# Kernel optimization log

Hardware: AMD Instinct MI355X
Metric: run time of the kernel (lower is better)

Reference implementation:

```python
import jax, jax.numpy as jnp
import numpy as np

N_HEADS = 16
ROPE_BASE = 10000.0


def _apply_rope(t, cos, sin):
    # t: (B, H, S, D); cos/sin: (S, D/2). Rotate-half convention.
    d2 = t.shape[-1] // 2
    t1, t2 = t[..., :d2], t[..., d2:]
    return jnp.concatenate([t1 * cos - t2 * sin, t2 * cos + t1 * sin], axis=-1)


def setup_inputs() -> dict:
    key = jax.random.key(0)
    k0, k1, k2, k3, k4 = jax.random.split(key, 5)
    B, S, E = 4, 2048, 1024
    scale = 0.02
    x = jax.random.normal(k0, (B, S, E), dtype=jnp.float32)
    w_qkv = jax.random.normal(k1, (E, 3 * E), dtype=jnp.float32) * scale
    b_qkv = jnp.zeros((3 * E,), dtype=jnp.float32)
    w_proj = jax.random.normal(k2, (E, E), dtype=jnp.float32) * scale
    b_proj = jnp.zeros((E,), dtype=jnp.float32)
    return {"x": x, "w_qkv": w_qkv, "b_qkv": b_qkv, "w_proj": w_proj, "b_proj": b_proj}


def reference(x, w_qkv, b_qkv, w_proj, b_proj):
    B, S, E = x.shape
    H = N_HEADS
    D = E // H
    # fused QKV projection
    qkv = x @ w_qkv + b_qkv                      # (B, S, 3E)
    q, k, v = jnp.split(qkv, 3, axis=-1)
    def to_heads(t):
        return t.reshape(B, S, H, D).transpose(0, 2, 1, 3)  # (B, H, S, D)
    q, k, v = to_heads(q), to_heads(k), to_heads(v)
    # RoPE (rotate-half)
    inv_freq = ROPE_BASE ** (-jnp.arange(0, D, 2, dtype=jnp.float32) / D)  # (D/2,)
    pos = jnp.arange(S, dtype=jnp.float32)
    freqs = pos[:, None] * inv_freq[None, :]     # (S, D/2)
    cos, sin = jnp.cos(freqs), jnp.sin(freqs)
    q = _apply_rope(q, cos, sin)
    k = _apply_rope(k, cos, sin)
    # causal SDPA
    scores = jnp.einsum('bhqd,bhkd->bhqk', q, k) / jnp.sqrt(jnp.float32(D))
    causal = jnp.tril(jnp.ones((S, S), dtype=bool))
    scores = jnp.where(causal, scores, jnp.float32(-1e30))
    probs = jax.nn.softmax(scores, axis=-1)
    out = jnp.einsum('bhqk,bhkd->bhqd', probs, v)  # (B, H, S, D)
    out = out.transpose(0, 2, 1, 3).reshape(B, S, E)
    # output projection (dropout is identity at p=0 / eval)
    return out @ w_proj + b_proj
```

## Files before the change

kernel.cpp:

```cpp
#include <hip/hip_runtime.h>

typedef unsigned short u16;
typedef __bf16 bf16x8 __attribute__((ext_vector_type(8)));
typedef float f32x4 __attribute__((ext_vector_type(4)));

__device__ __forceinline__ u16 f2b(float f) {
    unsigned u = __builtin_bit_cast(unsigned, f);
    unsigned r = (u + 0x7fffu + ((u >> 16) & 1u)) >> 16;
    return (u16)r;
}
#if __has_builtin(__builtin_amdgcn_cvt_pk_bf16_f32)
typedef __bf16 bf16x2_t __attribute__((ext_vector_type(2)));
__device__ __forceinline__ unsigned pk2(float a, float b) {
    return __builtin_bit_cast(unsigned, __builtin_amdgcn_cvt_pk_bf16_f32(a, b));
}
#else
__device__ __forceinline__ unsigned pk2(float a, float b) {
    return (unsigned)f2b(a) | ((unsigned)f2b(b) << 16);
}
#endif
#if __has_builtin(__builtin_amdgcn_exp2f)
#define EXP2F(x) __builtin_amdgcn_exp2f(x)
#else
#define EXP2F(x) exp2f(x)
#endif

__device__ __forceinline__ void gl_lds16(const u16* g, u16* l) {
    __builtin_amdgcn_global_load_lds(
        (const __attribute__((address_space(1))) unsigned*)(const void*)g,
        (__attribute__((address_space(3))) unsigned*)(void*)l, 16, 0, 0);
}

__global__ __launch_bounds__(256) void k_convert(const float* __restrict__ in,
                                                 u16* __restrict__ out, int n8) {
    int i = blockIdx.x * 256 + threadIdx.x;
    if (i >= n8) return;
    const float4* p = (const float4*)(in + (size_t)i * 8);
    float4 a = p[0], b = p[1];
    u16 t[8] = {f2b(a.x), f2b(a.y), f2b(a.z), f2b(a.w),
                f2b(b.x), f2b(b.y), f2b(b.z), f2b(b.w)};
    *(uint4*)(out + (size_t)i * 8) = *(const uint4*)t;
}

__global__ __launch_bounds__(256) void k_transpose_bf16(const float* __restrict__ in,
                                                        u16* __restrict__ out,
                                                        int R, int C) {
    __shared__ u16 tile[64][72];
    int tc = blockIdx.x * 64;
    int tr = blockIdx.y * 64;
    for (int i = threadIdx.x; i < 4096; i += 256) {
        int r = i >> 6, c = i & 63;
        tile[c][r] = f2b(in[(size_t)(tr + r) * C + tc + c]);
    }
    __syncthreads();
    for (int i = threadIdx.x; i < 4096; i += 256) {
        int r = i >> 6, c = i & 63;
        out[(size_t)(tc + r) * R + tr + c] = tile[r][c];
    }
}

__device__ __forceinline__ void gemm_mainloop(const u16* __restrict__ Ab,
                                              const u16* __restrict__ Bb, int K,
                                              u16* As, u16* Bs, int tid,
                                              f32x4 (&acc)[4][4]) {
    const int wave = tid >> 6, lane = tid & 63;
    const int col = lane & 15, quad = lane >> 4;
    const int wm = wave >> 1, wn = wave & 1;
    const int lrow = lane >> 2, lk = (lane & 3) * 8;
    u16* ldsA0 = As + (wave * 16) * 32;
    u16* ldsA1 = As + (64 + wave * 16) * 32;
    u16* ldsB0 = Bs + (wave * 16) * 32;
    u16* ldsB1 = Bs + (64 + wave * 16) * 32;
    const u16* gA0 = Ab + (size_t)(wave * 16 + lrow) * K + lk;
    const u16* gA1 = gA0 + (size_t)64 * K;
    const u16* gB0 = Bb + (size_t)(wave * 16 + lrow) * K + lk;
    const u16* gB1 = gB0 + (size_t)64 * K;
    for (int k0 = 0; k0 < K; k0 += 64) {
        if (k0) __syncthreads();
#pragma unroll
        for (int kh = 0; kh < 2; ++kh) {
            int ko = k0 + kh * 32;
            gl_lds16(gA0 + ko, ldsA0 + kh * 4096);
            gl_lds16(gA1 + ko, ldsA1 + kh * 4096);
            gl_lds16(gB0 + ko, ldsB0 + kh * 4096);
            gl_lds16(gB1 + ko, ldsB1 + kh * 4096);
        }
        __syncthreads();
#pragma unroll
        for (int kh = 0; kh < 2; ++kh) {
            bf16x8 af[4], bfr[4];
#pragma unroll
            for (int mt = 0; mt < 4; ++mt)
                af[mt] = *(const bf16x8*)(As + kh * 4096 +
                                          (wm * 64 + mt * 16 + col) * 32 + quad * 8);
#pragma unroll
            for (int nt = 0; nt < 4; ++nt)
                bfr[nt] = *(const bf16x8*)(Bs + kh * 4096 +
                                           (wn * 64 + nt * 16 + col) * 32 + quad * 8);
#pragma unroll
            for (int mt = 0; mt < 4; ++mt)
#pragma unroll
                for (int nt = 0; nt < 4; ++nt)
                    acc[mt][nt] = __builtin_amdgcn_mfma_f32_16x16x32_bf16(
                        af[mt], bfr[nt], acc[mt][nt], 0, 0, 0);
        }
    }
}

__global__ __launch_bounds__(256) void k_gemm_qkv_rope(
    const u16* __restrict__ A, const u16* __restrict__ Bt,
    const float* __restrict__ bias, u16* __restrict__ Qr, u16* __restrict__ Kr,
    u16* __restrict__ Vt) {
    __shared__ __align__(16) u16 As[2 * 128 * 32];
    __shared__ __align__(16) u16 Bs[2 * 128 * 32];
    const int K = 1024;
    int tid = threadIdx.x;
    int lane = tid & 63, wave = tid >> 6;
    int col = lane & 15, quad = lane >> 4;
    int wm = wave >> 1, wn = wave & 1;
    int mBase = blockIdx.y * 128;
    int nBase = blockIdx.x * 128;
    f32x4 acc[4][4] = {};
    gemm_mainloop(A + (size_t)mBase * K, Bt + (size_t)nBase * K, K, As, Bs, tid, acc);

    int n64 = nBase + wn * 64;
    int region = n64 >> 10;
    int h = (n64 & 1023) >> 6;
    if (region < 2) {
        u16* out = (region == 0) ? Qr : Kr;
        float qs = (region == 0) ? 0.18033688011112042f : 1.0f;
        const float C0 = 0.4152410118609203f;
#pragma unroll
        for (int nt = 0; nt < 2; ++nt) {
            int d1 = nt * 16 + col;
            float inv_freq = exp2f(-C0 * (float)d1);
            float b1 = bias[n64 + nt * 16 + col];
            float b2 = bias[n64 + nt * 16 + col + 32];
#pragma unroll
            for (int mt = 0; mt < 4; ++mt) {
                int mrow = mBase + wm * 64 + mt * 16 + quad * 4;
#pragma unroll
                for (int r = 0; r < 4; ++r) {
                    int m = mrow + r;
                    int s = m & 2047, b = m >> 11;
                    float sn, cs;
                    sincosf((float)s * inv_freq, &sn, &cs);
                    float t1 = acc[mt][nt][r] + b1;
                    float t2 = acc[mt][nt + 2][r] + b2;
                    size_t base = ((size_t)((b * 16 + h) * 2048 + s)) * 64;
                    out[base + d1] = f2b((t1 * cs - t2 * sn) * qs);
                    out[base + d1 + 32] = f2b((t2 * cs + t1 * sn) * qs);
                }
            }
        }
    } else {
#pragma unroll
        for (int nt = 0; nt < 4; ++nt) {
            int d = nt * 16 + col;
            float bv = bias[n64 + nt * 16 + col];
#pragma unroll
            for (int mt = 0; mt < 4; ++mt) {
                int mrow = mBase + wm * 64 + mt * 16 + quad * 4;
#pragma unroll
                for (int r = 0; r < 4; ++r) {
                    int m = mrow + r;
                    int s = m & 2047, b = m >> 11;
                    Vt[((size_t)((b * 16 + h) * 64 + d)) * 2048 + s] =
                        f2b(acc[mt][nt][r] + bv);
                }
            }
        }
    }
}

__global__ __launch_bounds__(256) void k_attn(const u16* __restrict__ Qr,
                                              const u16* __restrict__ Kr,
                                              const u16* __restrict__ Vt,
                                              u16* __restrict__ O) {
    __shared__ __align__(16) u16 Ks[64 * 72];
    __shared__ __align__(16) u16 Vs[64 * 72];
    int tid = threadIdx.x, wave = tid >> 6, lane = tid & 63;
    int col = lane & 15, quad = lane >> 4;
    int bx = blockIdx.x, bh = blockIdx.y;
    int b = bh >> 4, h = bh & 15;
    size_t headQ = (size_t)bh * 2048 * 64;
    size_t headV = (size_t)bh * 64 * 2048;
    int r0 = tid >> 3, kc = tid & 7;
    int rb72 = ((col >> 2) * 8 + (col & 3)) * 72;

    for (int half = 0; half < 2; ++half) {
        int qb = half ? bx : (15 - bx);
        int t0 = 2 * qb, t1 = t0 + 1;
        int myq0 = qb * 128 + wave * 16 + col;
        int myq1 = myq0 + 64;
        const u16* qp0 = Qr + headQ + (size_t)myq0 * 64;
        const u16* qp1 = Qr + headQ + (size_t)myq1 * 64;
        bf16x8 aq00 = *(const bf16x8*)(qp0 + quad * 8);
        bf16x8 aq01 = *(const bf16x8*)(qp0 + 32 + quad * 8);
        bf16x8 aq10 = *(const bf16x8*)(qp1 + quad * 8);
        bf16x8 aq11 = *(const bf16x8*)(qp1 + 32 + quad * 8);
        f32x4 o0[4] = {}, o1[4] = {};
        float l0 = 0.f, l1 = 0.f;

        for (int j = 0; j <= t1; ++j) {
            bool d0 = (j <= t0);
            __syncthreads();
            {
                const u16* kg = Kr + headQ + (size_t)(j * 64 + r0) * 64 + kc * 8;
                const u16* vg = Vt + headV + (size_t)r0 * 2048 + j * 64 + kc * 8;
                *(uint4*)(Ks + r0 * 72 + kc * 8) = *(const uint4*)kg;
                *(uint4*)(Ks + (r0 + 32) * 72 + kc * 8) = *(const uint4*)(kg + 32 * 64);
                *(uint4*)(Vs + r0 * 72 + kc * 8) = *(const uint4*)vg;
                *(uint4*)(Vs + (r0 + 32) * 72 + kc * 8) = *(const uint4*)(vg + 32 * 2048);
            }
            __syncthreads();
            f32x4 s0[4], s1[4];
#pragma unroll
            for (int nt = 0; nt < 4; ++nt) {
                const u16* kp = Ks + rb72 + ((nt & 1) * 32 + (nt >> 1) * 4) * 72;
                bf16x8 ak0 = *(const bf16x8*)(kp + quad * 8);
                bf16x8 ak1 = *(const bf16x8*)(kp + 32 + quad * 8);
                if (d0) {
                    f32x4 z = {};
                    z = __builtin_amdgcn_mfma_f32_16x16x32_bf16(ak0, aq00, z, 0, 0, 0);
                    s0[nt] = __builtin_amdgcn_mfma_f32_16x16x32_bf16(ak1, aq01, z, 0, 0, 0);
                }
                f32x4 z = {};
                z = __builtin_amdgcn_mfma_f32_16x16x32_bf16(ak0, aq10, z, 0, 0, 0);
                s1[nt] = __builtin_amdgcn_mfma_f32_16x16x32_bf16(ak1, aq11, z, 0, 0, 0);
            }
            if (j == t0) {
#pragma unroll
                for (int nt = 0; nt < 4; ++nt) {
                    int keyb = j * 64 + (nt & 1) * 32 + quad * 8 + (nt >> 1) * 4;
#pragma unroll
                    for (int r = 0; r < 4; ++r)
                        if (keyb + r > myq0) s0[nt][r] = -3.0e38f;
                }
            }
            if (j == t1) {
#pragma unroll
                for (int nt = 0; nt < 4; ++nt) {
                    int keyb = j * 64 + (nt & 1) * 32 + quad * 8 + (nt >> 1) * 4;
#pragma unroll
                    for (int r = 0; r < 4; ++r)
                        if (keyb + r > myq1) s1[nt][r] = -3.0e38f;
                }
            }
            unsigned P40[8], P41[8];
            if (d0) {
#pragma unroll
                for (int nt = 0; nt < 4; ++nt) {
                    float p0 = EXP2F(s0[nt][0]);
                    float p1 = EXP2F(s0[nt][1]);
                    float p2 = EXP2F(s0[nt][2]);
                    float p3 = EXP2F(s0[nt][3]);
                    l0 += (p0 + p1) + (p2 + p3);
                    P40[2 * nt] = pk2(p0, p1);
                    P40[2 * nt + 1] = pk2(p2, p3);
                }
            }
#pragma unroll
            for (int nt = 0; nt < 4; ++nt) {
                float p0 = EXP2F(s1[nt][0]);
                float p1 = EXP2F(s1[nt][1]);
                float p2 = EXP2F(s1[nt][2]);
                float p3 = EXP2F(s1[nt][3]);
                l1 += (p0 + p1) + (p2 + p3);
                P41[2 * nt] = pk2(p0, p1);
                P41[2 * nt + 1] = pk2(p2, p3);
            }
#pragma unroll
            for (int kk = 0; kk < 2; ++kk) {
                uint4 bw0, bw1;
                bw0.x = P40[2 * kk];
                bw0.y = P40[2 * kk + 1];
                bw0.z = P40[2 * kk + 4];
                bw0.w = P40[2 * kk + 5];
                bw1.x = P41[2 * kk];
                bw1.y = P41[2 * kk + 1];
                bw1.z = P41[2 * kk + 4];
                bw1.w = P41[2 * kk + 5];
                bf16x8 bp0 = __builtin_bit_cast(bf16x8, bw0);
                bf16x8 bp1 = __builtin_bit_cast(bf16x8, bw1);
#pragma unroll
                for (int mt = 0; mt < 4; ++mt) {
                    bf16x8 av = *(const bf16x8*)(Vs + (mt * 16 + col) * 72 + kk * 32 + quad * 8);
                    if (d0)
                        o0[mt] = __builtin_amdgcn_mfma_f32_16x16x32_bf16(av, bp0, o0[mt], 0, 0, 0);
                    o1[mt] = __builtin_amdgcn_mfma_f32_16x16x32_bf16(av, bp1, o1[mt], 0, 0, 0);
                }
            }
        }
        l0 += __shfl_xor(l0, 16);
        l0 += __shfl_xor(l0, 32);
        l1 += __shfl_xor(l1, 16);
        l1 += __shfl_xor(l1, 32);
        float inv0 = 1.0f / l0, inv1 = 1.0f / l1;
        u16* orow0 = O + (size_t)(b * 2048 + myq0) * 1024 + h * 64;
        u16* orow1 = O + (size_t)(b * 2048 + myq1) * 1024 + h * 64;
#pragma unroll
        for (int mt = 0; mt < 4; ++mt) {
            uint2 w0, w1;
            w0.x = pk2(o0[mt][0] * inv0, o0[mt][1] * inv0);
            w0.y = pk2(o0[mt][2] * inv0, o0[mt][3] * inv0);
            w1.x = pk2(o1[mt][0] * inv1, o1[mt][1] * inv1);
            w1.y = pk2(o1[mt][2] * inv1, o1[mt][3] * inv1);
            *(uint2*)(orow0 + mt * 16 + quad * 4) = w0;
            *(uint2*)(orow1 + mt * 16 + quad * 4) = w1;
        }
    }
}

__global__ __launch_bounds__(256) void k_gemm_proj(const u16* __restrict__ A,
                                                   const u16* __restrict__ Bt,
                                                   const float* __restrict__ bias,
                                                   float* __restrict__ out) {
    __shared__ __align__(16) u16 As[2 * 128 * 32];
    __shared__ __align__(16) u16 Bs[2 * 128 * 32];
    const int K = 1024;
    int tid = threadIdx.x;
    int lane = tid & 63, wave = tid >> 6;
    int col = lane & 15, quad = lane >> 4;
    int wm = wave >> 1, wn = wave & 1;
    int mBase = blockIdx.y * 128;
    int nBase = blockIdx.x * 128;
    f32x4 acc[4][4] = {};
    gemm_mainloop(A + (size_t)mBase * K, Bt + (size_t)nBase * K, K, As, Bs, tid, acc);
#pragma unroll
    for (int nt = 0; nt < 4; ++nt) {
        int n = nBase + wn * 64 + nt * 16 + col;
        float bv = bias[n];
#pragma unroll
        for (int mt = 0; mt < 4; ++mt) {
            int m = mBase + wm * 64 + mt * 16 + quad * 4;
#pragma unroll
            for (int r = 0; r < 4; ++r)
                out[(size_t)(m + r) * 1024 + n] = acc[mt][nt][r] + bv;
        }
    }
}

extern "C" void kernel_launch(void* const* d_in, const int* in_sizes, int n_in,
                              void* d_out, int out_size, void* d_ws, size_t ws_size,
                              hipStream_t stream) {
    const float* x = (const float*)d_in[0];
    const float* w_qkv = (const float*)d_in[1];
    const float* b_qkv = (const float*)d_in[2];
    const float* w_proj = (const float*)d_in[3];
    const float* b_proj = (const float*)d_in[4];
    float* out = (float*)d_out;
    char* ws = (char*)d_ws;
    u16* x_bf = (u16*)(ws);
    u16* wqkvT = (u16*)(ws + 16777216);
    u16* wprojT = (u16*)(ws + 23068672);
    u16* Qr = (u16*)(ws + 25165824);
    u16* Kr = (u16*)(ws + 41943040);
    u16* Vt = (u16*)(ws + 58720256);
    u16* AO = (u16*)(ws + 75497472);

    k_convert<<<4096, 256, 0, stream>>>(x, x_bf, 1048576);
    k_transpose_bf16<<<dim3(48, 16), 256, 0, stream>>>(w_qkv, wqkvT, 1024, 3072);
    k_transpose_bf16<<<dim3(16, 16), 256, 0, stream>>>(w_proj, wprojT, 1024, 1024);
    k_gemm_qkv_rope<<<dim3(24, 64), 256, 0, stream>>>(x_bf, wqkvT, b_qkv, Qr, Kr, Vt);
    k_attn<<<dim3(8, 64), 256, 0, stream>>>(Qr, Kr, Vt, AO);
    k_gemm_proj<<<dim3(8, 64), 256, 0, stream>>>(AO, wprojT, b_proj, out);
}
```

Baseline: 278.1 us.

## Double-buffer GEMM LDS loads and register-prefetch K/V tiles in attention

The GEMM mainloop now uses a two-stage LDS ping-pong with 32-wide k steps. Each iteration issues the next tile's global-to-LDS loads before computing on the current buffer, so load latency overlaps the MFMAs. The attention kernel prefetches the next K/V tile into registers while the current tile is being computed. The RoPE sincos call is swapped for the fast __sincosf intrinsic. Costs are more registers, and each GEMM k step now carries its own barrier with half the MFMA work, plus some precision loss in sin/cos at large positions.

```diff
diff --git a/kernel.cpp b/kernel.cpp
--- a/kernel.cpp
+++ b/kernel.cpp
@@ -67,43 +67,39 @@
     const int col = lane & 15, quad = lane >> 4;
     const int wm = wave >> 1, wn = wave & 1;
     const int lrow = lane >> 2, lk = (lane & 3) * 8;
-    u16* ldsA0 = As + (wave * 16) * 32;
-    u16* ldsA1 = As + (64 + wave * 16) * 32;
-    u16* ldsB0 = Bs + (wave * 16) * 32;
-    u16* ldsB1 = Bs + (64 + wave * 16) * 32;
+    const int wofs = wave * 512;
     const u16* gA0 = Ab + (size_t)(wave * 16 + lrow) * K + lk;
     const u16* gA1 = gA0 + (size_t)64 * K;
     const u16* gB0 = Bb + (size_t)(wave * 16 + lrow) * K + lk;
     const u16* gB1 = gB0 + (size_t)64 * K;
-    for (int k0 = 0; k0 < K; k0 += 64) {
-        if (k0) __syncthreads();
-#pragma unroll
-        for (int kh = 0; kh < 2; ++kh) {
-            int ko = k0 + kh * 32;
-            gl_lds16(gA0 + ko, ldsA0 + kh * 4096);
-            gl_lds16(gA1 + ko, ldsA1 + kh * 4096);
-            gl_lds16(gB0 + ko, ldsB0 + kh * 4096);
-            gl_lds16(gB1 + ko, ldsB1 + kh * 4096);
-        }
+    gl_lds16(gA0, As + wofs);
+    gl_lds16(gA1, As + 2048 + wofs);
+    gl_lds16(gB0, Bs + wofs);
+    gl_lds16(gB1, Bs + 2048 + wofs);
+    for (int k0 = 0; k0 < K; k0 += 32) {
+        const int cb = ((k0 >> 5) & 1) * 4096;
         __syncthreads();
-#pragma unroll
-        for (int kh = 0; kh < 2; ++kh) {
-            bf16x8 af[4], bfr[4];
-#pragma unroll
-            for (int mt = 0; mt < 4; ++mt)
-                af[mt] = *(const bf16x8*)(As + kh * 4096 +
-                                          (wm * 64 + mt * 16 + col) * 32 + quad * 8);
+        int kn = k0 + 32;
+        if (kn < K) {
+            const int nb = 4096 - cb;
+            gl_lds16(gA0 + kn, As + nb + wofs);
+            gl_lds16(gA1 + kn, As + nb + 2048 + wofs);
+            gl_lds16(gB0 + kn, Bs + nb + wofs);
+            gl_lds16(gB1 + kn, Bs + nb + 2048 + wofs);
+        }
+        bf16x8 af[4], bfr[4];
+#pragma unroll
+        for (int mt = 0; mt < 4; ++mt)
+            af[mt] = *(const bf16x8*)(As + cb + (wm * 64 + mt * 16 + col) * 32 + quad * 8);
+#pragma unroll
+        for (int nt = 0; nt < 4; ++nt)
+            bfr[nt] = *(const bf16x8*)(Bs + cb + (wn * 64 + nt * 16 + col) * 32 + quad * 8);
+#pragma unroll
+        for (int mt = 0; mt < 4; ++mt)
 #pragma unroll
             for (int nt = 0; nt < 4; ++nt)
-                bfr[nt] = *(const bf16x8*)(Bs + kh * 4096 +
-                                           (wn * 64 + nt * 16 + col) * 32 + quad * 8);
-#pragma unroll
-            for (int mt = 0; mt < 4; ++mt)
-#pragma unroll
-                for (int nt = 0; nt < 4; ++nt)
-                    acc[mt][nt] = __builtin_amdgcn_mfma_f32_16x16x32_bf16(
-                        af[mt], bfr[nt], acc[mt][nt], 0, 0, 0);
-        }
+                acc[mt][nt] = __builtin_amdgcn_mfma_f32_16x16x32_bf16(
+                    af[mt], bfr[nt], acc[mt][nt], 0, 0, 0);
     }
 }
 
@@ -144,7 +140,7 @@
                     int m = mrow + r;
                     int s = m & 2047, b = m >> 11;
                     float sn, cs;
-                    sincosf((float)s * inv_freq, &sn, &cs);
+                    __sincosf((float)s * inv_freq, &sn, &cs);
                     float t1 = acc[mt][nt][r] + b1;
                     float t2 = acc[mt][nt + 2][r] + b2;
                     size_t base = ((size_t)((b * 16 + h) * 2048 + s)) * 64;
@@ -187,6 +183,8 @@
     size_t headV = (size_t)bh * 64 * 2048;
     int r0 = tid >> 3, kc = tid & 7;
     int rb72 = ((col >> 2) * 8 + (col & 3)) * 72;
+    const u16* kgB = Kr + headQ + (size_t)r0 * 64 + kc * 8;
+    const u16* vgB = Vt + headV + (size_t)r0 * 2048 + kc * 8;
 
     for (int half = 0; half < 2; ++half) {
         int qb = half ? bx : (15 - bx);
@@ -202,18 +200,28 @@
         f32x4 o0[4] = {}, o1[4] = {};
         float l0 = 0.f, l1 = 0.f;
 
+        uint4 pk0 = *(const uint4*)(kgB);
+        uint4 pk1 = *(const uint4*)(kgB + (size_t)32 * 64);
+        uint4 pv0 = *(const uint4*)(vgB);
+        uint4 pv1 = *(const uint4*)(vgB + (size_t)32 * 2048);
+
         for (int j = 0; j <= t1; ++j) {
             bool d0 = (j <= t0);
             __syncthreads();
+            *(uint4*)(Ks + r0 * 72 + kc * 8) = pk0;
+            *(uint4*)(Ks + (r0 + 32) * 72 + kc * 8) = pk1;
+            *(uint4*)(Vs + r0 * 72 + kc * 8) = pv0;
+            *(uint4*)(Vs + (r0 + 32) * 72 + kc * 8) = pv1;
+            __syncthreads();
             {
-                const u16* kg = Kr + headQ + (size_t)(j * 64 + r0) * 64 + kc * 8;
-                const u16* vg = Vt + headV + (size_t)r0 * 2048 + j * 64 + kc * 8;
-                *(uint4*)(Ks + r0 * 72 + kc * 8) = *(const uint4*)kg;
-                *(uint4*)(Ks + (r0 + 32) * 72 + kc * 8) = *(const uint4*)(kg + 32 * 64);
-                *(uint4*)(Vs + r0 * 72 + kc * 8) = *(const uint4*)vg;
-                *(uint4*)(Vs + (r0 + 32) * 72 + kc * 8) = *(const uint4*)(vg + 32 * 2048);
-            }
-            __syncthreads();
+                int j2 = (j < t1) ? (j + 1) : t1;
+                const u16* kg = kgB + (size_t)(j2 * 64) * 64;
+                const u16* vg = vgB + (size_t)(j2 * 64);
+                pk0 = *(const uint4*)kg;
+                pk1 = *(const uint4*)(kg + (size_t)32 * 64);
+                pv0 = *(const uint4*)vg;
+                pv1 = *(const uint4*)(vg + (size_t)32 * 2048);
+            }
             f32x4 s0[4], s1[4];
 #pragma unroll
             for (int nt = 0; nt < 4; ++nt) {
```

Measured after the change: 284.2 us. 2.2% more time.
